# Performance work log

Measured on AMD Instinct MI355X. Metric: run time of the kernel, lower is better.

Reference implementation:

```python
import jax, jax.numpy as jnp
import numpy as np

N = 50000      # num_nodes
E = 1600000    # num_edges (avg degree 32)
F_IN = 512     # in_features
F_OUT = 64     # out_features
C = 4          # num_cores


def setup_inputs() -> dict:
    key = jax.random.key(0)
    ks = jax.random.split(key, 5)
    x = jax.random.normal(ks[0], (N, F_IN), jnp.float32)
    edge_index = jax.random.randint(ks[1], (2, E), 0, N, dtype=jnp.int32)
    # KokaoCore.signal modeled as tanh(w . v + b) -> scalar, one (w, b) per core
    core_w = jax.random.normal(ks[2], (C, F_IN), jnp.float32) / np.sqrt(F_IN)
    core_b = jnp.zeros((C,), jnp.float32)
    # output_transform: nn.Linear(num_cores, out_features)
    W_out = jax.random.normal(ks[3], (F_OUT, C), jnp.float32) / np.sqrt(C)
    b_out = jnp.zeros((F_OUT,), jnp.float32)
    return {"x": x, "edge_index": edge_index, "core_w": core_w,
            "core_b": core_b, "W_out": W_out, "b_out": b_out}


def reference(x, edge_index, core_w, core_b, W_out, b_out):
    src, tgt = edge_index[0], edge_index[1]
    # per-node, per-core scalar signal (computed once per node, gathered per edge)
    s = jnp.tanh(x @ core_w.T + core_b)                              # (N, C)
    seg_sum = jax.ops.segment_sum(s[src], tgt, num_segments=N)       # (N, C)
    count = jax.ops.segment_sum(jnp.ones((E,), x.dtype), tgt, num_segments=N)  # (N,)
    # mean over neighbors; nodes with no in-edges stay zero (torch.zeros init)
    avg = jnp.where(count[:, None] > 0, seg_sum / jnp.maximum(count, 1.0)[:, None], 0.0)
    # aggregated[i] = avg_signal * x[i][:out_features], stacked over cores on last dim
    messages = avg[:, None, :] * x[:, :F_OUT, None]                  # (N, F_OUT, C)
    out = jnp.einsum('nfc,oc->nfo', messages, W_out) + b_out         # (N, F_OUT, F_OUT)
    return jax.nn.relu(out)
```

## Files before the change

kernel.cpp:

```cpp
#include <hip/hip_runtime.h>

#define F_IN 512
#define F_OUT 64
#define CAP 128

typedef float v4f __attribute__((ext_vector_type(4)));
typedef int   v4i __attribute__((ext_vector_type(4)));

__global__ __launch_bounds__(256) void signal_kernel(
    const float* __restrict__ x, const float* __restrict__ core_w,
    const float* __restrict__ core_b, float* __restrict__ s,
    int* __restrict__ cursor, int N) {
  int wave = (int)((blockIdx.x * blockDim.x + threadIdx.x) >> 6);
  int lane = threadIdx.x & 63;
  if (wave >= N) return;

  const v4f* xv = (const v4f*)(x + (size_t)wave * F_IN);
  v4f a0 = xv[lane * 2];
  v4f a1 = xv[lane * 2 + 1];

  float p[4];
#pragma unroll
  for (int c = 0; c < 4; ++c) {
    const v4f* wv = (const v4f*)(core_w + c * F_IN);
    v4f w0 = wv[lane * 2];
    v4f w1 = wv[lane * 2 + 1];
    p[c] = a0.x * w0.x + a0.y * w0.y + a0.z * w0.z + a0.w * w0.w +
           a1.x * w1.x + a1.y * w1.y + a1.z * w1.z + a1.w * w1.w;
  }
#pragma unroll
  for (int off = 32; off > 0; off >>= 1) {
#pragma unroll
    for (int c = 0; c < 4; ++c) p[c] += __shfl_down(p[c], off, 64);
  }
  if (lane == 0) {
    v4f r;
    r.x = tanhf(p[0] + core_b[0]);
    r.y = tanhf(p[1] + core_b[1]);
    r.z = tanhf(p[2] + core_b[2]);
    r.w = tanhf(p[3] + core_b[3]);
    ((v4f*)s)[wave] = r;
    cursor[wave] = 0;
  }
}

__global__ __launch_bounds__(256) void fill_kernel(
    const int* __restrict__ src, const int* __restrict__ tgt,
    int* __restrict__ cursor, int* __restrict__ bsrc, int E) {
  int base = (int)(blockIdx.x * blockDim.x + threadIdx.x) * 4;
  if (base >= E) return;
  if (base + 3 < E) {
    v4i u = *(const v4i*)(src + base);
    v4i v = *(const v4i*)(tgt + base);
#pragma unroll
    for (int k = 0; k < 4; ++k) {
      int vv = v[k];
      int p = atomicAdd(&cursor[vv], 1);
      if (p < CAP) bsrc[(size_t)vv * CAP + p] = u[k];
    }
  } else {
    for (int k = 0; k < 4 && base + k < E; ++k) {
      int vv = tgt[base + k];
      int p = atomicAdd(&cursor[vv], 1);
      if (p < CAP) bsrc[(size_t)vv * CAP + p] = src[base + k];
    }
  }
}

__global__ __launch_bounds__(256) void out_kernel(
    const float* __restrict__ x, const float* __restrict__ s,
    const int* __restrict__ cursor, const int* __restrict__ bsrc,
    const float* __restrict__ W_out, const float* __restrict__ b_out,
    float* __restrict__ out, int N) {
  int lane = threadIdx.x & 63;
  int gwave = (int)((blockIdx.x * blockDim.x + threadIdx.x) >> 6);
  int nwaves = (int)((gridDim.x * blockDim.x) >> 6);
  int col = lane & 15;

  v4f w0 = ((const v4f*)W_out)[col * 4 + 0];
  v4f w1 = ((const v4f*)W_out)[col * 4 + 1];
  v4f w2 = ((const v4f*)W_out)[col * 4 + 2];
  v4f w3 = ((const v4f*)W_out)[col * 4 + 3];
  v4f bq = ((const v4f*)b_out)[col];

  for (int n = gwave; n < N; n += nwaves) {
    int deg = cursor[n];
    int m = min(deg, CAP);
    const int* bp = bsrc + (size_t)n * CAP;
    float a0 = 0.f, a1 = 0.f, a2 = 0.f, a3 = 0.f;
    for (int e = lane; e < m; e += 64) {
      int u = bp[e];
      v4f sv = ((const v4f*)s)[u];
      a0 += sv.x; a1 += sv.y; a2 += sv.z; a3 += sv.w;
    }
#pragma unroll
    for (int off = 1; off < 64; off <<= 1) {
      a0 += __shfl_xor(a0, off, 64);
      a1 += __shfl_xor(a1, off, 64);
      a2 += __shfl_xor(a2, off, 64);
      a3 += __shfl_xor(a3, off, 64);
    }
    float inv = deg > 0 ? 1.0f / (float)deg : 0.0f;
    a0 *= inv; a1 *= inv; a2 *= inv; a3 *= inv;

    float t0 = a0 * w0.x + a1 * w0.y + a2 * w0.z + a3 * w0.w;
    float t1 = a0 * w1.x + a1 * w1.y + a2 * w1.z + a3 * w1.w;
    float t2 = a0 * w2.x + a1 * w2.y + a2 * w2.z + a3 * w2.w;
    float t3 = a0 * w3.x + a1 * w3.y + a2 * w3.z + a3 * w3.w;

    float xval = x[(size_t)n * F_IN + lane];

    v4f* ov = (v4f*)(out + (size_t)n * (F_OUT * F_OUT));
#pragma unroll
    for (int it = 0; it < 16; ++it) {
      float xf = __shfl(xval, (lane >> 4) + it * 4, 64);
      v4f r;
      r.x = fmaxf(xf * t0 + bq.x, 0.0f);
      r.y = fmaxf(xf * t1 + bq.y, 0.0f);
      r.z = fmaxf(xf * t2 + bq.z, 0.0f);
      r.w = fmaxf(xf * t3 + bq.w, 0.0f);
      ov[lane + it * 64] = r;
    }
  }
}

extern "C" void kernel_launch(void* const* d_in, const int* in_sizes, int n_in,
                              void* d_out, int out_size, void* d_ws, size_t ws_size,
                              hipStream_t stream) {
  const float* x      = (const float*)d_in[0];
  const int*   eidx   = (const int*)d_in[1];
  const float* core_w = (const float*)d_in[2];
  const float* core_b = (const float*)d_in[3];
  const float* W_out  = (const float*)d_in[4];
  const float* b_out  = (const float*)d_in[5];
  float* out = (float*)d_out;

  const int N = in_sizes[0] / F_IN;
  const int E = in_sizes[1] / 2;
  const int* src = eidx;
  const int* tgt = eidx + E;

  float* s      = (float*)d_ws;
  int*   cursor = (int*)(s + (size_t)N * 4);
  int*   bsrc   = cursor + N;

  signal_kernel<<<(N + 3) / 4, 256, 0, stream>>>(x, core_w, core_b, s, cursor, N);
  {
    int threads = (E + 3) / 4;
    fill_kernel<<<(threads + 255) / 256, 256, 0, stream>>>(src, tgt, cursor, bsrc, E);
  }
  out_kernel<<<2048, 256, 0, stream>>>(x, s, cursor, bsrc, W_out, b_out, out, N);
}
```

Measured before the change: 1.049 ms.

## Fuse signal, bucket-fill and output stages into one cooperative kernel

Replaces the three separate launches with a single cooperative persistent kernel of 1024 blocks that runs the signal, edge-bucketing and output stages, separated by grid-wide syncs. The goal is to remove the launch gaps and tail effects between kernels. In exchange the grid is smaller than the original launches, and grid.sync has its own cost. The old three-kernel path is kept as a fallback if the cooperative launch fails.

```diff
diff --git a/kernel.cpp b/kernel.cpp
--- a/kernel.cpp
+++ b/kernel.cpp
@@ -1,4 +1,7 @@
 #include <hip/hip_runtime.h>
+#include <hip/hip_cooperative_groups.h>
+
+namespace cg = cooperative_groups;
 
 #define F_IN 512
 #define F_OUT 64
@@ -6,6 +9,120 @@
 
 typedef float v4f __attribute__((ext_vector_type(4)));
 typedef int   v4i __attribute__((ext_vector_type(4)));
+
+__global__ __launch_bounds__(256, 4) void fused_kernel(
+    const float* __restrict__ x, const int* __restrict__ src,
+    const int* __restrict__ tgt, const float* __restrict__ core_w,
+    const float* __restrict__ core_b, const float* __restrict__ W_out,
+    const float* __restrict__ b_out, float* __restrict__ s,
+    int* __restrict__ cursor, int* __restrict__ bsrc,
+    float* __restrict__ out, int N, int E) {
+  cg::grid_group grid = cg::this_grid();
+  const int tid = threadIdx.x;
+  const int lane = tid & 63;
+  const int gthread = (int)(blockIdx.x * blockDim.x + tid);
+  const int nthreads = (int)(gridDim.x * blockDim.x);
+  const int gwave = gthread >> 6;
+  const int nwaves = nthreads >> 6;
+
+  for (int n = gwave; n < N; n += nwaves) {
+    const v4f* xv = (const v4f*)(x + (size_t)n * F_IN);
+    v4f a0 = xv[lane * 2];
+    v4f a1 = xv[lane * 2 + 1];
+    float p[4];
+#pragma unroll
+    for (int c = 0; c < 4; ++c) {
+      const v4f* wv = (const v4f*)(core_w + c * F_IN);
+      v4f w0 = wv[lane * 2];
+      v4f w1 = wv[lane * 2 + 1];
+      p[c] = a0.x * w0.x + a0.y * w0.y + a0.z * w0.z + a0.w * w0.w +
+             a1.x * w1.x + a1.y * w1.y + a1.z * w1.z + a1.w * w1.w;
+    }
+#pragma unroll
+    for (int off = 32; off > 0; off >>= 1) {
+#pragma unroll
+      for (int c = 0; c < 4; ++c) p[c] += __shfl_down(p[c], off, 64);
+    }
+    if (lane == 0) {
+      v4f r;
+      r.x = tanhf(p[0] + core_b[0]);
+      r.y = tanhf(p[1] + core_b[1]);
+      r.z = tanhf(p[2] + core_b[2]);
+      r.w = tanhf(p[3] + core_b[3]);
+      ((v4f*)s)[n] = r;
+      cursor[n] = 0;
+    }
+  }
+  grid.sync();
+
+  const int nq = E >> 2;
+  for (int q = gthread; q < nq; q += nthreads) {
+    int base = q * 4;
+    v4i u = *(const v4i*)(src + base);
+    v4i v = *(const v4i*)(tgt + base);
+#pragma unroll
+    for (int k = 0; k < 4; ++k) {
+      int vv = v[k];
+      int p = atomicAdd(&cursor[vv], 1);
+      if (p < CAP) bsrc[(size_t)vv * CAP + p] = u[k];
+    }
+  }
+  if (gthread == 0) {
+    for (int e = nq * 4; e < E; ++e) {
+      int vv = tgt[e];
+      int p = atomicAdd(&cursor[vv], 1);
+      if (p < CAP) bsrc[(size_t)vv * CAP + p] = src[e];
+    }
+  }
+  grid.sync();
+
+  const int col = lane & 15;
+  v4f w0 = ((const v4f*)W_out)[col * 4 + 0];
+  v4f w1 = ((const v4f*)W_out)[col * 4 + 1];
+  v4f w2 = ((const v4f*)W_out)[col * 4 + 2];
+  v4f w3 = ((const v4f*)W_out)[col * 4 + 3];
+  v4f bq = ((const v4f*)b_out)[col];
+
+  for (int n = gwave; n < N; n += nwaves) {
+    int deg = cursor[n];
+    int m = min(deg, CAP);
+    const int* bp = bsrc + (size_t)n * CAP;
+    float a0 = 0.f, a1 = 0.f, a2 = 0.f, a3 = 0.f;
+    for (int e = lane; e < m; e += 64) {
+      int u = bp[e];
+      v4f sv = ((const v4f*)s)[u];
+      a0 += sv.x; a1 += sv.y; a2 += sv.z; a3 += sv.w;
+    }
+#pragma unroll
+    for (int off = 1; off < 64; off <<= 1) {
+      a0 += __shfl_xor(a0, off, 64);
+      a1 += __shfl_xor(a1, off, 64);
+      a2 += __shfl_xor(a2, off, 64);
+      a3 += __shfl_xor(a3, off, 64);
+    }
+    float inv = deg > 0 ? 1.0f / (float)deg : 0.0f;
+    a0 *= inv; a1 *= inv; a2 *= inv; a3 *= inv;
+
+    float t0 = a0 * w0.x + a1 * w0.y + a2 * w0.z + a3 * w0.w;
+    float t1 = a0 * w1.x + a1 * w1.y + a2 * w1.z + a3 * w1.w;
+    float t2 = a0 * w2.x + a1 * w2.y + a2 * w2.z + a3 * w2.w;
+    float t3 = a0 * w3.x + a1 * w3.y + a2 * w3.z + a3 * w3.w;
+
+    float xval = x[(size_t)n * F_IN + lane];
+
+    v4f* ov = (v4f*)(out + (size_t)n * (F_OUT * F_OUT));
+#pragma unroll
+    for (int it = 0; it < 16; ++it) {
+      float xf = __shfl(xval, (lane >> 4) + it * 4, 64);
+      v4f r;
+      r.x = fmaxf(xf * t0 + bq.x, 0.0f);
+      r.y = fmaxf(xf * t1 + bq.y, 0.0f);
+      r.z = fmaxf(xf * t2 + bq.z, 0.0f);
+      r.w = fmaxf(xf * t3 + bq.w, 0.0f);
+      ov[lane + it * 64] = r;
+    }
+  }
+}
 
 __global__ __launch_bounds__(256) void signal_kernel(
     const float* __restrict__ x, const float* __restrict__ core_w,
@@ -14,11 +131,9 @@
   int wave = (int)((blockIdx.x * blockDim.x + threadIdx.x) >> 6);
   int lane = threadIdx.x & 63;
   if (wave >= N) return;
-
   const v4f* xv = (const v4f*)(x + (size_t)wave * F_IN);
   v4f a0 = xv[lane * 2];
   v4f a1 = xv[lane * 2 + 1];
-
   float p[4];
 #pragma unroll
   for (int c = 0; c < 4; ++c) {
@@ -76,13 +191,11 @@
   int gwave = (int)((blockIdx.x * blockDim.x + threadIdx.x) >> 6);
   int nwaves = (int)((gridDim.x * blockDim.x) >> 6);
   int col = lane & 15;
-
   v4f w0 = ((const v4f*)W_out)[col * 4 + 0];
   v4f w1 = ((const v4f*)W_out)[col * 4 + 1];
   v4f w2 = ((const v4f*)W_out)[col * 4 + 2];
   v4f w3 = ((const v4f*)W_out)[col * 4 + 3];
   v4f bq = ((const v4f*)b_out)[col];
-
   for (int n = gwave; n < N; n += nwaves) {
     int deg = cursor[n];
     int m = min(deg, CAP);
@@ -102,14 +215,11 @@
     }
     float inv = deg > 0 ? 1.0f / (float)deg : 0.0f;
     a0 *= inv; a1 *= inv; a2 *= inv; a3 *= inv;
-
     float t0 = a0 * w0.x + a1 * w0.y + a2 * w0.z + a3 * w0.w;
     float t1 = a0 * w1.x + a1 * w1.y + a2 * w1.z + a3 * w1.w;
     float t2 = a0 * w2.x + a1 * w2.y + a2 * w2.z + a3 * w2.w;
     float t3 = a0 * w3.x + a1 * w3.y + a2 * w3.z + a3 * w3.w;
-
     float xval = x[(size_t)n * F_IN + lane];
-
     v4f* ov = (v4f*)(out + (size_t)n * (F_OUT * F_OUT));
 #pragma unroll
     for (int it = 0; it < 16; ++it) {
@@ -135,8 +245,8 @@
   const float* b_out  = (const float*)d_in[5];
   float* out = (float*)d_out;
 
-  const int N = in_sizes[0] / F_IN;
-  const int E = in_sizes[1] / 2;
+  int N = in_sizes[0] / F_IN;
+  int E = in_sizes[1] / 2;
   const int* src = eidx;
   const int* tgt = eidx + E;
 
@@ -144,10 +254,16 @@
   int*   cursor = (int*)(s + (size_t)N * 4);
   int*   bsrc   = cursor + N;
 
-  signal_kernel<<<(N + 3) / 4, 256, 0, stream>>>(x, core_w, core_b, s, cursor, N);
-  {
+  void* args[] = {(void*)&x, (void*)&src, (void*)&tgt, (void*)&core_w,
+                  (void*)&core_b, (void*)&W_out, (void*)&b_out,
+                  (void*)&s, (void*)&cursor, (void*)&bsrc,
+                  (void*)&out, (void*)&N, (void*)&E};
+  hipError_t err = hipLaunchCooperativeKernel((void*)fused_kernel, dim3(1024),
+                                              dim3(256), args, 0, stream);
+  if (err != hipSuccess) {
+    signal_kernel<<<(N + 3) / 4, 256, 0, stream>>>(x, core_w, core_b, s, cursor, N);
     int threads = (E + 3) / 4;
     fill_kernel<<<(threads + 255) / 256, 256, 0, stream>>>(src, tgt, cursor, bsrc, E);
-  }
-  out_kernel<<<2048, 256, 0, stream>>>(x, s, cursor, bsrc, W_out, b_out, out, N);
-}
+    out_kernel<<<2048, 256, 0, stream>>>(x, s, cursor, bsrc, W_out, b_out, out, N);
+  }
+}
```

After: 1.249 ms. 1.19x slower.

## Replace neighbor bucket lists with fixed-point packed 64-bit atomic segment sums

Applied to the files above, without the earlier changes.

Instead of building per-target neighbor lists and gathering signals in the output kernel, the fill kernel quantizes each source signal to fixed point and accumulates packed sums plus the degree into two 64-bit atomics per target node. The output kernel then decodes the mean directly, with no gather or wave reduction. This removes the CAP-sized bucket array and the scattered gathers. The trade-off is quantization error: the fourth channel and the degree share a word at reduced precision (17 fractional bits), and packed fields could overflow for very high degrees.

```diff
diff --git a/kernel.cpp b/kernel.cpp
--- a/kernel.cpp
+++ b/kernel.cpp
@@ -2,15 +2,17 @@
 
 #define F_IN 512
 #define F_OUT 64
-#define CAP 128
 
 typedef float v4f __attribute__((ext_vector_type(4)));
 typedef int   v4i __attribute__((ext_vector_type(4)));
+typedef unsigned int uint32;
+typedef unsigned long long u64;
+
 
 __global__ __launch_bounds__(256) void signal_kernel(
     const float* __restrict__ x, const float* __restrict__ core_w,
     const float* __restrict__ core_b, float* __restrict__ s,
-    int* __restrict__ cursor, int N) {
+    u64* __restrict__ segA, u64* __restrict__ segB, int N) {
   int wave = (int)((blockIdx.x * blockDim.x + threadIdx.x) >> 6);
   int lane = threadIdx.x & 63;
   if (wave >= N) return;
@@ -40,13 +42,15 @@
     r.z = tanhf(p[2] + core_b[2]);
     r.w = tanhf(p[3] + core_b[3]);
     ((v4f*)s)[wave] = r;
-    cursor[wave] = 0;
+    segA[wave] = 0ull;
+    segB[wave] = 0ull;
   }
 }
 
 __global__ __launch_bounds__(256) void fill_kernel(
     const int* __restrict__ src, const int* __restrict__ tgt,
-    int* __restrict__ cursor, int* __restrict__ bsrc, int E) {
+    const float* __restrict__ s, u64* __restrict__ segA,
+    u64* __restrict__ segB, int E) {
   int base = (int)(blockIdx.x * blockDim.x + threadIdx.x) * 4;
   if (base >= E) return;
   if (base + 3 < E) {
@@ -54,24 +58,37 @@
     v4i v = *(const v4i*)(tgt + base);
 #pragma unroll
     for (int k = 0; k < 4; ++k) {
+      v4f sv = ((const v4f*)s)[u[k]];
+      uint32 q0 = (uint32)__float2int_rn((sv.x + 1.0f) * 8388608.0f);
+      uint32 q1 = (uint32)__float2int_rn((sv.y + 1.0f) * 8388608.0f);
+      uint32 q2 = (uint32)__float2int_rn((sv.z + 1.0f) * 8388608.0f);
+      uint32 q3 = (uint32)__float2int_rn((sv.w + 1.0f) * 131072.0f);
+      u64 e0 = (u64)q0 | ((u64)q1 << 32);
+      u64 e1 = (u64)q2 | ((u64)(q3 | (1u << 25)) << 32);
       int vv = v[k];
-      int p = atomicAdd(&cursor[vv], 1);
-      if (p < CAP) bsrc[(size_t)vv * CAP + p] = u[k];
+      atomicAdd(&segA[vv], e0);
+      atomicAdd(&segB[vv], e1);
     }
   } else {
     for (int k = 0; k < 4 && base + k < E; ++k) {
+      v4f sv = ((const v4f*)s)[src[base + k]];
+      uint32 q0 = (uint32)__float2int_rn((sv.x + 1.0f) * 8388608.0f);
+      uint32 q1 = (uint32)__float2int_rn((sv.y + 1.0f) * 8388608.0f);
+      uint32 q2 = (uint32)__float2int_rn((sv.z + 1.0f) * 8388608.0f);
+      uint32 q3 = (uint32)__float2int_rn((sv.w + 1.0f) * 131072.0f);
+      u64 e0 = (u64)q0 | ((u64)q1 << 32);
+      u64 e1 = (u64)q2 | ((u64)(q3 | (1u << 25)) << 32);
       int vv = tgt[base + k];
-      int p = atomicAdd(&cursor[vv], 1);
-      if (p < CAP) bsrc[(size_t)vv * CAP + p] = src[base + k];
+      atomicAdd(&segA[vv], e0);
+      atomicAdd(&segB[vv], e1);
     }
   }
 }
 
 __global__ __launch_bounds__(256) void out_kernel(
-    const float* __restrict__ x, const float* __restrict__ s,
-    const int* __restrict__ cursor, const int* __restrict__ bsrc,
-    const float* __restrict__ W_out, const float* __restrict__ b_out,
-    float* __restrict__ out, int N) {
+    const float* __restrict__ x, const u64* __restrict__ segA,
+    const u64* __restrict__ segB, const float* __restrict__ W_out,
+    const float* __restrict__ b_out, float* __restrict__ out, int N) {
   int lane = threadIdx.x & 63;
   int gwave = (int)((blockIdx.x * blockDim.x + threadIdx.x) >> 6);
   int nwaves = (int)((gridDim.x * blockDim.x) >> 6);
@@ -84,24 +101,20 @@
   v4f bq = ((const v4f*)b_out)[col];
 
   for (int n = gwave; n < N; n += nwaves) {
-    int deg = cursor[n];
-    int m = min(deg, CAP);
-    const int* bp = bsrc + (size_t)n * CAP;
-    float a0 = 0.f, a1 = 0.f, a2 = 0.f, a3 = 0.f;
-    for (int e = lane; e < m; e += 64) {
-      int u = bp[e];
-      v4f sv = ((const v4f*)s)[u];
-      a0 += sv.x; a1 += sv.y; a2 += sv.z; a3 += sv.w;
-    }
-#pragma unroll
-    for (int off = 1; off < 64; off <<= 1) {
-      a0 += __shfl_xor(a0, off, 64);
-      a1 += __shfl_xor(a1, off, 64);
-      a2 += __shfl_xor(a2, off, 64);
-      a3 += __shfl_xor(a3, off, 64);
-    }
-    float inv = deg > 0 ? 1.0f / (float)deg : 0.0f;
-    a0 *= inv; a1 *= inv; a2 *= inv; a3 *= inv;
+    u64 wa = segA[n];
+    u64 wb = segB[n];
+    uint32 lo0 = (uint32)wa;
+    uint32 hi0 = (uint32)(wa >> 32);
+    uint32 lo1 = (uint32)wb;
+    uint32 hi1 = (uint32)(wb >> 32);
+    uint32 deg = hi1 >> 25;
+    uint32 f3  = hi1 & 0x1ffffffu;
+    float fdeg = (float)deg;
+    float inv = deg ? 1.0f / fdeg : 0.0f;
+    float a0 = ((float)lo0 * 0x1p-23f - fdeg) * inv;
+    float a1 = ((float)hi0 * 0x1p-23f - fdeg) * inv;
+    float a2 = ((float)lo1 * 0x1p-23f - fdeg) * inv;
+    float a3 = ((float)f3  * 0x1p-17f - fdeg) * inv;
 
     float t0 = a0 * w0.x + a1 * w0.y + a2 * w0.z + a3 * w0.w;
     float t1 = a0 * w1.x + a1 * w1.y + a2 * w1.z + a3 * w1.w;
@@ -140,14 +153,14 @@
   const int* src = eidx;
   const int* tgt = eidx + E;
 
-  float* s      = (float*)d_ws;
-  int*   cursor = (int*)(s + (size_t)N * 4);
-  int*   bsrc   = cursor + N;
+  float* s    = (float*)d_ws;
+  u64*   segA = (u64*)(s + (size_t)N * 4);
+  u64*   segB = segA + N;
 
-  signal_kernel<<<(N + 3) / 4, 256, 0, stream>>>(x, core_w, core_b, s, cursor, N);
+  signal_kernel<<<(N + 3) / 4, 256, 0, stream>>>(x, core_w, core_b, s, segA, segB, N);
   {
     int threads = (E + 3) / 4;
-    fill_kernel<<<(threads + 255) / 256, 256, 0, stream>>>(src, tgt, cursor, bsrc, E);
+    fill_kernel<<<(threads + 255) / 256, 256, 0, stream>>>(src, tgt, s, segA, segB, E);
   }
-  out_kernel<<<2048, 256, 0, stream>>>(x, s, cursor, bsrc, W_out, b_out, out, N);
+  out_kernel<<<2048, 256, 0, stream>>>(x, segA, segB, W_out, b_out, out, N);
 }
```

Result: no change. 1.034 ms (-1.4%).

## Replace per-node atomic bucketing with block-level partition and shared-memory fixed-point aggregation

Applied to the files above, without the earlier changes.

Edges are now partitioned into buckets of 256 target nodes using a shared-memory histogram, so each block issues one global atomic per bucket instead of one per edge. A separate aggregation kernel then accumulates neighbour signals per bucket in LDS, using offset fixed-point integer atomics, and writes a per-node average. The output kernel reads only the precomputed average, which removes the gather and reduction from the store-bound pass. The change adds a kernel launch and quantises the signals to 2^-23 precision. Bucket capacity is fixed at 10240, so a bucket with more edges than that would silently drop them.

```diff
diff --git a/kernel.cpp b/kernel.cpp
--- a/kernel.cpp
+++ b/kernel.cpp
@@ -2,15 +2,21 @@
 
 #define F_IN 512
 #define F_OUT 64
-#define CAP 128
+#define NB_SHIFT 8
+#define CAP_B 10240
+#define P_CHUNK 4096
 
 typedef float v4f __attribute__((ext_vector_type(4)));
 typedef int   v4i __attribute__((ext_vector_type(4)));
+typedef unsigned int uint32;
+
 
 __global__ __launch_bounds__(256) void signal_kernel(
     const float* __restrict__ x, const float* __restrict__ core_w,
     const float* __restrict__ core_b, float* __restrict__ s,
-    int* __restrict__ cursor, int N) {
+    uint32* __restrict__ gcur, int N, int nb) {
+  if (blockIdx.x == 0 && threadIdx.x < (unsigned)nb) gcur[threadIdx.x] = 0;
+
   int wave = (int)((blockIdx.x * blockDim.x + threadIdx.x) >> 6);
   int lane = threadIdx.x & 63;
   if (wave >= N) return;
@@ -40,36 +46,93 @@
     r.z = tanhf(p[2] + core_b[2]);
     r.w = tanhf(p[3] + core_b[3]);
     ((v4f*)s)[wave] = r;
-    cursor[wave] = 0;
-  }
-}
-
-__global__ __launch_bounds__(256) void fill_kernel(
+  }
+}
+
+__global__ __launch_bounds__(256) void part_kernel(
     const int* __restrict__ src, const int* __restrict__ tgt,
-    int* __restrict__ cursor, int* __restrict__ bsrc, int E) {
-  int base = (int)(blockIdx.x * blockDim.x + threadIdx.x) * 4;
-  if (base >= E) return;
-  if (base + 3 < E) {
-    v4i u = *(const v4i*)(src + base);
-    v4i v = *(const v4i*)(tgt + base);
-#pragma unroll
-    for (int k = 0; k < 4; ++k) {
-      int vv = v[k];
-      int p = atomicAdd(&cursor[vv], 1);
-      if (p < CAP) bsrc[(size_t)vv * CAP + p] = u[k];
+    uint32* __restrict__ gcur, uint32* __restrict__ grec, int E, int nb) {
+  __shared__ uint32 hist[256];
+  __shared__ uint32 cur[256];
+  int tid = threadIdx.x;
+  int start = (int)blockIdx.x * P_CHUNK;
+
+  if (tid < nb) hist[tid] = 0;
+  __syncthreads();
+
+  int b[16];
+  uint32 rec[16];
+#pragma unroll
+  for (int j = 0; j < 16; ++j) {
+    int i = start + j * 256 + tid;
+    b[j] = -1;
+    rec[j] = 0;
+    if (i < E) {
+      int u = src[i];
+      int v = tgt[i];
+      b[j] = v >> NB_SHIFT;
+      rec[j] = (uint32)(v & 255) | ((uint32)u << 8);
+      atomicAdd(&hist[b[j]], 1u);
     }
-  } else {
-    for (int k = 0; k < 4 && base + k < E; ++k) {
-      int vv = tgt[base + k];
-      int p = atomicAdd(&cursor[vv], 1);
-      if (p < CAP) bsrc[(size_t)vv * CAP + p] = src[base + k];
+  }
+  __syncthreads();
+  if (tid < nb) {
+    uint32 tot = hist[tid];
+    cur[tid] = tot ? atomicAdd(&gcur[tid], tot) : 0u;
+  }
+  __syncthreads();
+#pragma unroll
+  for (int j = 0; j < 16; ++j) {
+    if (b[j] >= 0) {
+      uint32 pos = atomicAdd(&cur[b[j]], 1u);
+      if (pos < CAP_B) grec[(size_t)b[j] * CAP_B + pos] = rec[j];
     }
   }
 }
 
+__global__ __launch_bounds__(256) void agg_kernel(
+    const float* __restrict__ s, const uint32* __restrict__ gcur,
+    const uint32* __restrict__ grec, float* __restrict__ avg, int N) {
+  int b = blockIdx.x;
+  int tid = threadIdx.x;
+  __shared__ uint32 acc[256 * 5];
+
+#pragma unroll
+  for (int k = 0; k < 5; ++k) acc[tid + k * 256] = 0;
+  __syncthreads();
+
+  uint32 cnt = gcur[b];
+  if (cnt > CAP_B) cnt = CAP_B;
+  const uint32* rp = grec + (size_t)b * CAP_B;
+  for (uint32 r = tid; r < cnt; r += 256) {
+    uint32 rec = rp[r];
+    uint32 node = rec & 255u;
+    uint32 u = rec >> 8;
+    v4f sv = ((const v4f*)s)[u];
+    atomicAdd(&acc[node        ], (uint32)__float2int_rn((sv.x + 1.0f) * 8388608.0f));
+    atomicAdd(&acc[node +  256 ], (uint32)__float2int_rn((sv.y + 1.0f) * 8388608.0f));
+    atomicAdd(&acc[node +  512 ], (uint32)__float2int_rn((sv.z + 1.0f) * 8388608.0f));
+    atomicAdd(&acc[node +  768 ], (uint32)__float2int_rn((sv.w + 1.0f) * 8388608.0f));
+    atomicAdd(&acc[node + 1024 ], 1u);
+  }
+  __syncthreads();
+
+  int n = (b << NB_SHIFT) | tid;
+  if (n < N) {
+    uint32 deg = acc[tid + 1024];
+    float fdeg = (float)deg;
+    float inv = deg ? 1.0f / fdeg : 0.0f;
+    v4f a;
+    a.x = ((float)acc[tid       ] * 0x1p-23f - fdeg) * inv;
+    a.y = ((float)acc[tid +  256] * 0x1p-23f - fdeg) * inv;
+    a.z = ((float)acc[tid +  512] * 0x1p-23f - fdeg) * inv;
+    a.w = ((float)acc[tid +  768] * 0x1p-23f - fdeg) * inv;
+    ((v4f*)avg)[n] = a;
+  }
+}
+
 __global__ __launch_bounds__(256) void out_kernel(
-    const float* __restrict__ x, const float* __restrict__ s,
-    const int* __restrict__ cursor, const int* __restrict__ bsrc,
+    const float* __restrict__ x, const float* __restrict__ avg,
     const float* __restrict__ W_out, const float* __restrict__ b_out,
     float* __restrict__ out, int N) {
   int lane = threadIdx.x & 63;
@@ -84,29 +147,12 @@
   v4f bq = ((const v4f*)b_out)[col];
 
   for (int n = gwave; n < N; n += nwaves) {
-    int deg = cursor[n];
-    int m = min(deg, CAP);
-    const int* bp = bsrc + (size_t)n * CAP;
-    float a0 = 0.f, a1 = 0.f, a2 = 0.f, a3 = 0.f;
-    for (int e = lane; e < m; e += 64) {
-      int u = bp[e];
-      v4f sv = ((const v4f*)s)[u];
-      a0 += sv.x; a1 += sv.y; a2 += sv.z; a3 += sv.w;
-    }
-#pragma unroll
-    for (int off = 1; off < 64; off <<= 1) {
-      a0 += __shfl_xor(a0, off, 64);
-      a1 += __shfl_xor(a1, off, 64);
-      a2 += __shfl_xor(a2, off, 64);
-      a3 += __shfl_xor(a3, off, 64);
-    }
-    float inv = deg > 0 ? 1.0f / (float)deg : 0.0f;
-    a0 *= inv; a1 *= inv; a2 *= inv; a3 *= inv;
-
-    float t0 = a0 * w0.x + a1 * w0.y + a2 * w0.z + a3 * w0.w;
-    float t1 = a0 * w1.x + a1 * w1.y + a2 * w1.z + a3 * w1.w;
-    float t2 = a0 * w2.x + a1 * w2.y + a2 * w2.z + a3 * w2.w;
-    float t3 = a0 * w3.x + a1 * w3.y + a2 * w3.z + a3 * w3.w;
+    v4f a = ((const v4f*)avg)[n];
+
+    float t0 = a.x * w0.x + a.y * w0.y + a.z * w0.z + a.w * w0.w;
+    float t1 = a.x * w1.x + a.y * w1.y + a.z * w1.z + a.w * w1.w;
+    float t2 = a.x * w2.x + a.y * w2.y + a.z * w2.z + a.w * w2.w;
+    float t3 = a.x * w3.x + a.y * w3.y + a.z * w3.z + a.w * w3.w;
 
     float xval = x[(size_t)n * F_IN + lane];
 
@@ -139,15 +185,18 @@
   const int E = in_sizes[1] / 2;
   const int* src = eidx;
   const int* tgt = eidx + E;
-
-  float* s      = (float*)d_ws;
-  int*   cursor = (int*)(s + (size_t)N * 4);
-  int*   bsrc   = cursor + N;
-
-  signal_kernel<<<(N + 3) / 4, 256, 0, stream>>>(x, core_w, core_b, s, cursor, N);
+  const int nb = (N + 255) >> NB_SHIFT;
+
+  float*  s    = (float*)d_ws;
+  float*  avg  = s + (size_t)N * 4;
+  uint32* gcur = (uint32*)(avg + (size_t)N * 4);
+  uint32* grec = gcur + 256;
+
+  signal_kernel<<<(N + 3) / 4, 256, 0, stream>>>(x, core_w, core_b, s, gcur, N, nb);
   {
-    int threads = (E + 3) / 4;
-    fill_kernel<<<(threads + 255) / 256, 256, 0, stream>>>(src, tgt, cursor, bsrc, E);
-  }
-  out_kernel<<<2048, 256, 0, stream>>>(x, s, cursor, bsrc, W_out, b_out, out, N);
-}
+    int blocks = (E + P_CHUNK - 1) / P_CHUNK;
+    part_kernel<<<blocks, 256, 0, stream>>>(src, tgt, gcur, grec, E, nb);
+  }
+  agg_kernel<<<nb, 256, 0, stream>>>(s, gcur, grec, avg, N);
+  out_kernel<<<2048, 256, 0, stream>>>(x, avg, W_out, b_out, out, N);
+}
```

Result: faster. 927.1 us (-11.6%).
